# Optimization experiments

Measured on AMD Instinct MI355X. Metric: run time of the kernel, lower is better.

## Reference

```python
import jax, jax.numpy as jnp
import numpy as np

EPS = 1e-5
K = 32          # nsample in PCT sample_and_group
S1, S2 = 512, 256


def _bn_relu(h, gamma, beta, axes):
    # BatchNorm1d in training mode: batch stats over (batch, length) per channel (last axis here)
    mu = jnp.mean(h, axes, keepdims=True)
    var = jnp.var(h, axes, keepdims=True)
    return jax.nn.relu((h - mu) * jax.lax.rsqrt(var + EPS) * gamma + beta)


def _index_points(points, idx):
    # points [B,N,C], idx [B,...] int -> [B,...,C]
    return jax.vmap(lambda p, i: p[i])(points, idx)


def _fps(xyz, npoint):
    # farthest point sampling; deterministic start at index 0. xyz [B,N,3] -> [B,npoint] int32
    B, N, _ = xyz.shape

    def body(carry, _):
        dmin, far = carry
        c = jnp.take_along_axis(xyz, far[:, None, None], axis=1)  # [B,1,3]
        dmin = jnp.minimum(dmin, jnp.sum((xyz - c) ** 2, -1))     # [B,N]
        return (dmin, jnp.argmax(dmin, -1).astype(jnp.int32)), far

    init = (jnp.full((B, N), 1e10, xyz.dtype), jnp.zeros((B,), jnp.int32))
    _, idxs = jax.lax.scan(body, init, None, length=npoint)
    return jnp.transpose(idxs)  # [B, npoint]


def _sg(features, xyz, s, w1, g1, b1, w2, g2, b2):
    # features [B,N,C], xyz [B,N,3] -> (new_xyz [B,s,3], out [B,s,out_ch])
    xyz_c = jax.lax.stop_gradient(xyz)
    fps_idx = _fps(xyz_c, s)                       # [B,s]
    new_xyz = _index_points(xyz, fps_idx)          # [B,s,3]
    new_pts = _index_points(features, fps_idx)     # [B,s,C]
    q = jax.lax.stop_gradient(new_xyz)
    # squared distances centers->all points, [B,s,N]
    d = (jnp.sum(q * q, -1)[:, :, None] + jnp.sum(xyz_c * xyz_c, -1)[:, None, :]
         - 2.0 * jnp.einsum('bsc,bnc->bsn', q, xyz_c))
    _, knn = jax.lax.top_k(-d, K)                  # [B,s,K] nearest neighbors
    grouped = _index_points(features, knn)         # [B,s,K,C]
    rel = grouped - new_pts[:, :, None, :]
    feat = jnp.concatenate([rel, jnp.broadcast_to(new_pts[:, :, None, :], rel.shape)], -1)  # [B,s,K,2C]
    h = _bn_relu(jnp.einsum('bskc,oc->bsko', feat, w1), g1, b1, (0, 1, 2))
    h = _bn_relu(jnp.einsum('bskc,oc->bsko', h, w2), g2, b2, (0, 1, 2))
    return new_xyz, jnp.max(h, axis=2)             # max over K neighbors -> [B,s,out]


def _forward(x, w1, g1, b1, w2, g2, b2,
             s1_w1, s1_g1, s1_b1, s1_w2, s1_g2, s1_b2,
             s2_w1, s2_g1, s2_b1, s2_w2, s2_g2, s2_b2):
    xyz = jnp.transpose(x, (0, 2, 1))                                # [B,N,3]
    f = _bn_relu(jnp.einsum('bcn,oc->bno', x, w1), g1, b1, (0, 1))   # [B,N,64]
    f = _bn_relu(jnp.einsum('bnc,oc->bno', f, w2), g2, b2, (0, 1))   # [B,N,64]
    xyz1, f1 = _sg(f, xyz, S1, s1_w1, s1_g1, s1_b1, s1_w2, s1_g2, s1_b2)   # [B,512,128]
    _, f2 = _sg(f1, xyz1, S2, s2_w1, s2_g1, s2_b1, s2_w2, s2_g2, s2_b2)    # [B,256,256]
    return jnp.transpose(f2, (0, 2, 1))                              # [B,256,256] channel-first


def setup_inputs() -> dict:
    key = jax.random.key(0)
    ks = jax.random.split(key, 8)
    B, N = 32, 4096
    inp = {"x": jax.random.normal(ks[0], (B, 3, N), jnp.float32)}

    def w(k, o, i):
        return jax.random.normal(k, (o, i), jnp.float32) * (1.0 / np.sqrt(i))

    inp["w1"] = w(ks[1], 64, 3);   inp["g1"] = jnp.ones((64,), jnp.float32);  inp["b1"] = jnp.zeros((64,), jnp.float32)
    inp["w2"] = w(ks[2], 64, 64);  inp["g2"] = jnp.ones((64,), jnp.float32);  inp["b2"] = jnp.zeros((64,), jnp.float32)
    inp["s1_w1"] = w(ks[3], 128, 128); inp["s1_g1"] = jnp.ones((128,), jnp.float32); inp["s1_b1"] = jnp.zeros((128,), jnp.float32)
    inp["s1_w2"] = w(ks[4], 128, 128); inp["s1_g2"] = jnp.ones((128,), jnp.float32); inp["s1_b2"] = jnp.zeros((128,), jnp.float32)
    inp["s2_w1"] = w(ks[5], 256, 256); inp["s2_g1"] = jnp.ones((256,), jnp.float32); inp["s2_b1"] = jnp.zeros((256,), jnp.float32)
    inp["s2_w2"] = w(ks[6], 256, 256); inp["s2_g2"] = jnp.ones((256,), jnp.float32); inp["s2_b2"] = jnp.zeros((256,), jnp.float32)
    return inp


def reference(x, w1, g1, b1, w2, g2, b2,
              s1_w1, s1_g1, s1_b1, s1_w2, s1_g2, s1_b2,
              s2_w1, s2_g1, s2_b1, s2_w2, s2_g2, s2_b2):
    return _forward(x, w1, g1, b1, w2, g2, b2,
                    s1_w1, s1_g1, s1_b1, s1_w2, s1_g2, s1_b2,
                    s2_w1, s2_g1, s2_b1, s2_w2, s2_g2, s2_b2)
```

## Files before the change

kernel.cpp:

```cpp
#include <hip/hip_runtime.h>

typedef short short8 __attribute__((ext_vector_type(8)));
typedef _Float16 h8 __attribute__((ext_vector_type(8)));
typedef float f32x4 __attribute__((ext_vector_type(4)));

#define DEVI __device__ __forceinline__

DEVI float h2f(short s) { return (float)__builtin_bit_cast(_Float16, s); }
DEVI short f2h(float f) { return __builtin_bit_cast(short, (_Float16)f); }
DEVI f32x4 mfma16(short8 a, short8 b, f32x4 c) {
  return __builtin_amdgcn_mfma_f32_16x16x32_f16(
      __builtin_bit_cast(h8, a), __builtin_bit_cast(h8, b), c, 0, 0, 0);
}

DEVI float wave_max_bcast(float v) {
  const int ID = 0xff800000;
  int x = __builtin_bit_cast(int, v);
#define STEPM(ctrl)                                                     \
  {                                                                     \
    int t = __builtin_amdgcn_update_dpp(ID, x, ctrl, 0xf, 0xf, false);  \
    x = __builtin_bit_cast(int, fmaxf(__builtin_bit_cast(float, x),     \
                                      __builtin_bit_cast(float, t)));   \
  }
  STEPM(0x111) STEPM(0x112) STEPM(0x114) STEPM(0x118) STEPM(0x142) STEPM(0x143)
#undef STEPM
  return __builtin_bit_cast(float, __builtin_amdgcn_readlane(x, 63));
}
DEVI float wave_min_bcast_f(float v) {
  const int ID = 0x7f800000;
  int x = __builtin_bit_cast(int, v);
#define STEPN(ctrl)                                                     \
  {                                                                     \
    int t = __builtin_amdgcn_update_dpp(ID, x, ctrl, 0xf, 0xf, false);  \
    x = __builtin_bit_cast(int, fminf(__builtin_bit_cast(float, x),     \
                                      __builtin_bit_cast(float, t)));   \
  }
  STEPN(0x111) STEPN(0x112) STEPN(0x114) STEPN(0x118) STEPN(0x142) STEPN(0x143)
#undef STEPN
  return __builtin_bit_cast(float, __builtin_amdgcn_readlane(x, 63));
}
DEVI unsigned wave_min_bcast_u(unsigned v) {
  const int ID = (int)0xffffffff;
  int x = (int)v;
#define STEPU(ctrl)                                                     \
  {                                                                     \
    int t = __builtin_amdgcn_update_dpp(ID, x, ctrl, 0xf, 0xf, false);  \
    x = (int)((unsigned)x < (unsigned)t ? (unsigned)x : (unsigned)t);   \
  }
  STEPU(0x111) STEPU(0x112) STEPU(0x114) STEPU(0x118) STEPU(0x142) STEPU(0x143)
#undef STEPU
  return (unsigned)__builtin_amdgcn_readlane(x, 63);
}
DEVI unsigned wave_iscan_add(unsigned v) {
  int x = (int)v, t;
  t = __builtin_amdgcn_update_dpp(0, x, 0x111, 0xf, 0xf, false); x += t;
  t = __builtin_amdgcn_update_dpp(0, x, 0x112, 0xf, 0xf, false); x += t;
  t = __builtin_amdgcn_update_dpp(0, x, 0x114, 0xf, 0xf, false); x += t;
  t = __builtin_amdgcn_update_dpp(0, x, 0x118, 0xf, 0xf, false); x += t;
  t = __builtin_amdgcn_update_dpp(0, x, 0x142, 0xa, 0xf, false); x += t;
  t = __builtin_amdgcn_update_dpp(0, x, 0x143, 0xc, 0xf, false); x += t;
  return (unsigned)x;
}

__global__ __launch_bounds__(256) void prep_kernel(
    const float* __restrict__ w2, const float* __restrict__ s1w2,
    const float* __restrict__ s2w2, const float* __restrict__ s1w1,
    const float* __restrict__ s2w1, short* __restrict__ w2b,
    short* __restrict__ s1w2b, short* __restrict__ s2w2b,
    short* __restrict__ W1pp, short* __restrict__ W2pp) {
  int i = blockIdx.x * 256 + threadIdx.x;
  if (i < 4096) {
    w2b[i] = f2h(w2[i]);
  } else if (i < 20480) {
    int j = i - 4096; s1w2b[j] = f2h(s1w2[j]);
  } else if (i < 86016) {
    int j = i - 20480; s2w2b[j] = f2h(s2w2[j]);
  } else if (i < 102400) {
    int j = i - 86016; int c = j & 127;
    float v = s1w1[j]; if (c >= 64) v -= s1w1[j - 64];
    W1pp[j] = f2h(v);
  } else if (i < 167936) {
    int j = i - 102400; int c = j & 255;
    float v = s2w1[j]; if (c >= 128) v -= s2w1[j - 128];
    W2pp[j] = f2h(v);
  }
}

__global__ __launch_bounds__(256) void stageA_kernel(
    const float* __restrict__ x, const float* __restrict__ w1,
    float* __restrict__ xyz, short* __restrict__ h0) {
  int i = blockIdx.x * 256 + threadIdx.x;
  int b = i >> 12, n = i & 4095;
  const float* xb = x + ((size_t)b * 3 << 12) + n;
  float x0 = xb[0], x1 = xb[4096], x2 = xb[8192];
  float* xp = xyz + (size_t)i * 3;
  xp[0] = x0; xp[1] = x1; xp[2] = x2;
  short* hp = h0 + ((size_t)i << 6);
#pragma unroll
  for (int o8 = 0; o8 < 8; ++o8) {
    short8 t;
#pragma unroll
    for (int j = 0; j < 8; ++j) {
      int o = o8 * 8 + j;
      float h = x0 * w1[o * 3] + x1 * w1[o * 3 + 1] + x2 * w1[o * 3 + 2];
      t[j] = f2h(h);
    }
    *reinterpret_cast<short8*>(hp + o8 * 8) = t;
  }
}


DEVI void stats64_body(int bid, int nb, int tid, const short* __restrict__ h,
                       float* __restrict__ partials, int M) {
  __shared__ float l0[256], l1[256];
  const int c = tid & 63, g = tid >> 6;
  float s0 = 0.f, s1 = 0.f;
  for (int m = bid * 4 + g; m < M; m += nb * 4) {
    float v = h2f(h[(size_t)m * 64 + c]);
    s0 += v; s1 += v * v;
  }
  l0[tid] = s0; l1[tid] = s1;
  __syncthreads();
  if (g == 0) {
    for (int w = 1; w < 4; ++w) { s0 += l0[c + w * 64]; s1 += l1[c + w * 64]; }
    partials[(size_t)c * nb + bid] = s0;
    partials[(size_t)(64 + c) * nb + bid] = s1;
  }
}

DEVI void reduce2_body(int c, int tid, const float* __restrict__ partials,
                       const float* __restrict__ gamma, const float* __restrict__ beta,
                       float* __restrict__ scale, float* __restrict__ shift,
                       int NB, int C, float invM) {
  __shared__ float l0[4], l1[4];
  const float* p0 = partials + (size_t)c * NB;
  const float* p1 = partials + (size_t)(C + c) * NB;
  float s0 = 0.f, s1 = 0.f;
  for (int i = tid; i < NB; i += 256) { s0 += p0[i]; s1 += p1[i]; }
#pragma unroll
  for (int off = 1; off < 64; off <<= 1) {
    s0 += __shfl_xor(s0, off);
    s1 += __shfl_xor(s1, off);
  }
  if ((tid & 63) == 0) { l0[tid >> 6] = s0; l1[tid >> 6] = s1; }
  __syncthreads();
  if (tid == 0) {
    s0 = l0[0] + l0[1] + l0[2] + l0[3];
    s1 = l1[0] + l1[1] + l1[2] + l1[3];
    float mean = s0 * invM;
    float var = fmaxf(s1 * invM - mean * mean, 0.f);
    float sc = gamma[c] / sqrtf(var + 1e-5f);
    scale[c] = sc;
    shift[c] = beta[c] - mean * sc;
  }
}

__global__ __launch_bounds__(256) void reduce2_kernel(
    const float* __restrict__ partials, const float* __restrict__ gamma,
    const float* __restrict__ beta, float* __restrict__ scale,
    float* __restrict__ shift, int NB, int C, float invM) {
  reduce2_body(blockIdx.x, threadIdx.x, partials, gamma, beta, scale, shift, NB, C, invM);
}

DEVI void apply_body(int bid, int tid, const short* __restrict__ h,
                     short* __restrict__ f, const float* __restrict__ scale,
                     const float* __restrict__ shift) {
  size_t i = ((size_t)bid * 256 + tid) * 8;
  int c0 = (int)(i & 63);
  short8 v = *reinterpret_cast<const short8*>(h + i);
  short8 o;
#pragma unroll
  for (int j = 0; j < 8; ++j) {
    float y = h2f(v[j]) * scale[c0 + j] + shift[c0 + j];
    o[j] = f2h(fmaxf(y, 0.f));
  }
  *reinterpret_cast<short8*>(f + i) = o;
}

template <int NPTS, int T>
DEVI void fps_seg_body(char* smemraw, int bid, int tid, const float* __restrict__ xyz,
                       int* __restrict__ out, float* __restrict__ xyzc, int nsel,
                       int it0, int it1, float* __restrict__ dming,
                       int* __restrict__ farg) {
  __builtin_amdgcn_s_setprio(1);
  constexpr int PT = NPTS / T;
  constexpr int NW = T / 64;
  float* sx = (float*)smemraw;
  float* sy = sx + NPTS;
  float* sz = sy + NPTS;
  float* wv = sz + NPTS;
  unsigned* wi = (unsigned*)(wv + 2 * NW);
  const int lane = tid & 63, wave = tid >> 6;
  const float* base = xyz + (size_t)bid * NPTS * 3;
  float px[PT], py[PT], pz[PT], dmin[PT];
#pragma unroll
  for (int j = 0; j < PT; ++j) {
    int n = j * T + tid;
    px[j] = base[n * 3]; py[j] = base[n * 3 + 1]; pz[j] = base[n * 3 + 2];
    sx[n] = px[j]; sy[n] = py[j]; sz[n] = pz[j];
  }
  int far;
  if (it0 == 0) {
#pragma unroll
    for (int j = 0; j < PT; ++j) dmin[j] = 1e10f;
    far = 0;
  } else {
#pragma unroll
    for (int j = 0; j < PT; ++j) dmin[j] = dming[(size_t)bid * NPTS + j * T + tid];
    far = farg[bid];
  }
  __syncthreads();
  float cx = sx[far], cy = sy[far], cz = sz[far];
  for (int it = it0; it < it1; ++it) {
    if (tid == 0) {
      out[bid * nsel + it] = far;
      if (xyzc) {
        float* xc = xyzc + ((size_t)bid * nsel + it) * 3;
        xc[0] = cx; xc[1] = cy; xc[2] = cz;
      }
    }
    float bv = -1.f;
#pragma unroll
    for (int j = 0; j < PT; ++j) {
      float dx = __fsub_rn(px[j], cx), dy = __fsub_rn(py[j], cy), dz = __fsub_rn(pz[j], cz);
      float d = __fadd_rn(__fadd_rn(__fmul_rn(dx, dx), __fmul_rn(dy, dy)), __fmul_rn(dz, dz));
      float dm = fminf(dmin[j], d);
      dmin[j] = dm;
      bv = fmaxf(bv, dm);
    }
    float wmv = wave_max_bcast(bv);
    unsigned ci = 0xffffffffu;
#pragma unroll
    for (int j = PT - 1; j >= 0; --j)
      if (dmin[j] == wmv) ci = (unsigned)(j * T + tid);
    unsigned wmi = wave_min_bcast_u(ci);
    const int bsel = it & 1;
    if (lane == 0) { wv[bsel * NW + wave] = wmv; wi[bsel * NW + wave] = wmi; }
    __syncthreads();
    const int e = lane & (NW - 1);
    float v = wv[bsel * NW + e];
    unsigned si = wi[bsel * NW + e];
#define CMB(ctrl)                                                                        \
  {                                                                                      \
    float v2 = __builtin_bit_cast(                                                       \
        float, __builtin_amdgcn_update_dpp(0, __builtin_bit_cast(int, v), ctrl, 0xf, 0xf, true)); \
    unsigned i2 = (unsigned)__builtin_amdgcn_update_dpp(0, (int)si, ctrl, 0xf, 0xf, true);\
    bool bt = (v2 > v) || (v2 == v && i2 < si);                                          \
    v = bt ? v2 : v; si = bt ? i2 : si;                                                  \
  }
    if constexpr (NW >= 2) CMB(0x121)
    if constexpr (NW >= 4) CMB(0x122)
    if constexpr (NW >= 8) CMB(0x124)
#undef CMB
    far = (int)si;
    cx = sx[far]; cy = sy[far]; cz = sz[far];
  }
  if (it1 < nsel) {
#pragma unroll
    for (int j = 0; j < PT; ++j) dming[(size_t)bid * NPTS + j * T + tid] = dmin[j];
    if (tid == 0) farg[bid] = far;
  }
}

#define KNN_SMEM_BYTES ((4096 + 256 + 4 + 256 + 256) * 4)
template <int NPTS, int S>
DEVI void knn_body(char* smemraw, int bs, int tid, const float* __restrict__ pts,
                   const int* __restrict__ fpsidx, int* __restrict__ knn) {
  constexpr int PT = NPTS / 256;
  unsigned* hist = (unsigned*)smemraw;
  unsigned* csums = hist + 4096;
  unsigned* meta = csums + 256;
  float* bval = (float*)(meta + 4);
  unsigned* bidx = (unsigned*)(bval + 256);
  const int lane = tid & 63, wave = tid >> 6;
  const int b = bs / S;
  const int cidx = fpsidx[bs];
  const float* cp = pts + ((size_t)b * NPTS + cidx) * 3;
  const float qx = cp[0], qy = cp[1], qz = cp[2];
  const float qq = __fadd_rn(__fadd_rn(__fmul_rn(qx, qx), __fmul_rn(qy, qy)), __fmul_rn(qz, qz));
  const float* base = pts + (size_t)b * NPTS * 3;
  float d[PT]; unsigned u[PT];
#pragma unroll
  for (int j = 0; j < PT; ++j) {
    int n = j * 256 + tid;
    float x = base[n * 3], y = base[n * 3 + 1], z = base[n * 3 + 2];
    float pp = __fadd_rn(__fadd_rn(__fmul_rn(x, x), __fmul_rn(y, y)), __fmul_rn(z, z));
    float dot = __fadd_rn(__fadd_rn(__fmul_rn(qx, x), __fmul_rn(qy, y)), __fmul_rn(qz, z));
    d[j] = __fsub_rn(__fadd_rn(qq, pp), __fmul_rn(2.f, dot));
    unsigned bits = __builtin_bit_cast(unsigned, d[j]);
    unsigned m = (unsigned)((int)bits >> 31);
    u[j] = bits ^ (m | 0x80000000u);
  }
  {
    uint4 z4 = {0u, 0u, 0u, 0u};
    uint4* hq = (uint4*)hist;
    for (int i = tid; i < 1024; i += 256) hq[i] = z4;
    if (tid == 0) { meta[0] = 0; meta[3] = 0; }
  }
  __syncthreads();
#pragma unroll
  for (int j = 0; j < PT; ++j) atomicAdd(&hist[u[j] >> 20], 1u);
  __syncthreads();
  {
    const uint4* hq = (const uint4*)(hist + tid * 16);
    unsigned cs = 0;
#pragma unroll
    for (int q = 0; q < 4; ++q) {
      uint4 v = hq[q];
      cs += v.x + v.y + v.z + v.w;
    }
    csums[tid] = cs;
  }
  __syncthreads();
  if (wave == 0) {
    const int t4 = lane * 4;
    unsigned c0 = csums[t4], c1 = csums[t4 + 1], c2 = csums[t4 + 2], c3 = csums[t4 + 3];
    unsigned lt = c0 + c1 + c2 + c3;
    unsigned incl = wave_iscan_add(lt);
    unsigned excl = incl - lt;
    unsigned long long blt = __ballot(incl >= 32u);
    int L = __ffsll((long long)blt) - 1;
    if (lane == L) {
      unsigned cum = excl;
      int bucket = -1;
      unsigned cc[4] = {c0, c1, c2, c3};
#pragma unroll
      for (int q = 0; q < 4; ++q) {
        if (bucket < 0 && cum + cc[q] >= 32u) {
          int bbase = (t4 + q) * 16;
          for (int h = 0; h < 16; ++h) {
            unsigned hv = hist[bbase + h];
            if (cum + hv >= 32u) { bucket = bbase + h; break; }
            cum += hv;
          }
        } else if (bucket < 0) {
          cum += cc[q];
        }
      }
      meta[1] = (unsigned)bucket;
      meta[2] = cum;
    }
  }
  __syncthreads();
  const unsigned B = meta[1];
  const unsigned cb = meta[2];
  int* kout = knn + (size_t)bs * 32;
#pragma unroll
  for (int j = 0; j < PT; ++j) {
    unsigned bk = u[j] >> 20;
    if (bk < B) {
      unsigned p = atomicAdd(&meta[0], 1u);
      kout[p] = j * 256 + tid;
    } else if (bk == B) {
      unsigned p = atomicAdd(&meta[3], 1u);
      if (p < 256u) { bval[p] = d[j]; bidx[p] = (unsigned)(j * 256 + tid); }
    }
  }
  __syncthreads();
  const int m = 32 - (int)cb;
  if (wave == 0 && m > 0) {
    unsigned nb = meta[3]; if (nb > 256u) nb = 256u;
    float v0 = (lane < (int)nb) ? bval[lane] : 3.4e38f;
    unsigned i0 = (lane < (int)nb) ? bidx[lane] : 0xffffffffu;
    float v1 = (lane + 64 < (int)nb) ? bval[lane + 64] : 3.4e38f;
    unsigned i1 = (lane + 64 < (int)nb) ? bidx[lane + 64] : 0xffffffffu;
    float v2 = (lane + 128 < (int)nb) ? bval[lane + 128] : 3.4e38f;
    unsigned i2 = (lane + 128 < (int)nb) ? bidx[lane + 128] : 0xffffffffu;
    float v3 = (lane + 192 < (int)nb) ? bval[lane + 192] : 3.4e38f;
    unsigned i3 = (lane + 192 < (int)nb) ? bidx[lane + 192] : 0xffffffffu;
    for (int k = 0; k < m; ++k) {
      float lv = v0; unsigned li = i0;
      if (v1 < lv || (v1 == lv && i1 < li)) { lv = v1; li = i1; }
      if (v2 < lv || (v2 == lv && i2 < li)) { lv = v2; li = i2; }
      if (v3 < lv || (v3 == lv && i3 < li)) { lv = v3; li = i3; }
      float wmv = wave_min_bcast_f(lv);
      unsigned ci = (lv == wmv) ? li : 0xffffffffu;
      unsigned wmi = wave_min_bcast_u(ci);
      if (lane == 0) kout[cb + k] = (int)wmi;
      if (i0 == wmi) { v0 = 3.4e38f; i0 = 0xffffffffu; }
      if (i1 == wmi) { v1 = 3.4e38f; i1 = 0xffffffffu; }
      if (i2 == wmi) { v2 = 3.4e38f; i2 = 0xffffffffu; }
      if (i3 == wmi) { v3 = 3.4e38f; i3 = 0xffffffffu; }
    }
  }
}

template <int KD, int ND, bool GATHER, bool BNA, int NPTS, int S>
DEVI void gemm_body(char* smemraw, int bid, int tid, int gemmBlocks,
                    const short* A, const int* KNNp, const int* FPSp,
                    const short* __restrict__ W, const float* __restrict__ bnscale,
                    const float* __restrict__ bnshift, short* Hout,
                    float* __restrict__ partials) {
  constexpr int C = KD / 2;
  constexpr int NT = (ND > 128) ? 8 : ND / 16;
  constexpr int BR = (ND > 128) ? 64 : 128;
  constexpr int KC = (ND >= 256) ? 64 : KD;
  constexpr int LOG2KC = (KC == 64) ? 6 : 7;
  constexpr int NCH = KD / KC;
  constexpr int KTC = KC / 32;
  constexpr int LROW = KC + 8;
  short* lb = (short*)smemraw;
  float* lstats = (float*)(smemraw + ND * LROW * 2);
  const int wave = tid >> 6, lane = tid & 63;
  const int rowOff = (ND > 128) ? (wave >> 1) * 32 : wave * 32;
  const int colOff = (ND > 128) ? (wave & 1) * 128 : 0;
  const int mBase = bid * BR + rowOff;
  for (int i = tid; i < 2 * ND; i += 256) lstats[i] = 0.f;

  const short* aptr[2][2];
#pragma unroll
  for (int rg = 0; rg < 2; ++rg) {
    int m = mBase + rg * 16 + (lane & 15);
    if constexpr (GATHER) {
      int idx = KNNp[m];
      int bb = m / (S * 32);
      int s = (m - bb * (S * 32)) >> 5;
      int fidx = FPSp[bb * S + s];
      aptr[rg][0] = A + ((size_t)bb * NPTS + idx) * C;
      aptr[rg][1] = A + ((size_t)bb * NPTS + fidx) * C;
    } else {
      aptr[rg][0] = A + (size_t)m * KD;
      aptr[rg][1] = A + (size_t)m * KD + C;
    }
  }
  const int koLane = (lane >> 4) * 8;
  f32x4 acc[2][NT];
#pragma unroll
  for (int rg = 0; rg < 2; ++rg)
#pragma unroll
    for (int nt = 0; nt < NT; ++nt) acc[rg][nt] = (f32x4){0.f, 0.f, 0.f, 0.f};

#pragma unroll
  for (int ch = 0; ch < NCH; ++ch) {
    __syncthreads();
    constexpr int SIT = (ND * KC) / 2048;
#pragma unroll
    for (int i = 0; i < SIT; ++i) {
      int e = i * 2048 + tid * 8;
      int n = e >> LOG2KC, kk = e & (KC - 1);
      short8 v = *reinterpret_cast<const short8*>(W + (size_t)n * KD + ch * KC + kk);
      *reinterpret_cast<short8*>(&lb[n * LROW + kk]) = v;
    }
    __syncthreads();
#pragma unroll
    for (int ktc = 0; ktc < KTC; ++ktc) {
      const int kt = ch * KTC + ktc;
      const int half = (kt * 32 >= C) ? 1 : 0;
      const int ko = kt * 32 + koLane;
      const int koh = ko - half * C;
      short8 afrag[2];
#pragma unroll
      for (int rg = 0; rg < 2; ++rg) {
        short8 a = *reinterpret_cast<const short8*>(aptr[rg][half] + koh);
        if constexpr (BNA) {
          const float* scp = bnscale + ko;
          const float* shp = bnshift + ko;
#pragma unroll
          for (int j = 0; j < 8; ++j) {
            float v = h2f(a[j]);
            v = fmaxf(v * scp[j] + shp[j], 0.f);
            a[j] = f2h(v);
          }
        }
        afrag[rg] = a;
      }
#pragma unroll
      for (int nt = 0; nt < NT; ++nt) {
        short8 bfr = *reinterpret_cast<const short8*>(
            &lb[(colOff + nt * 16 + (lane & 15)) * LROW + ktc * 32 + koLane]);
        acc[0][nt] = mfma16(afrag[0], bfr, acc[0][nt]);
        acc[1][nt] = mfma16(afrag[1], bfr, acc[1][nt]);
      }
    }
  }
  __syncthreads();

#pragma unroll
  for (int nt = 0; nt < NT; ++nt) {
    float s0 = 0.f, s1 = 0.f;
#pragma unroll
    for (int rg = 0; rg < 2; ++rg)
#pragma unroll
      for (int i = 0; i < 4; ++i) {
        float v = acc[rg][nt][i];
        s0 += v; s1 += v * v;
      }
    s0 += __shfl_xor(s0, 16); s0 += __shfl_xor(s0, 32);
    s1 += __shfl_xor(s1, 16); s1 += __shfl_xor(s1, 32);
    if (lane < 16) {
      atomicAdd(&lstats[colOff + nt * 16 + lane], s0);
      atomicAdd(&lstats[ND + colOff + nt * 16 + lane], s1);
    }
  }
#pragma unroll
  for (int rg = 0; rg < 2; ++rg)
#pragma unroll
    for (int nt = 0; nt < NT; ++nt)
#pragma unroll
      for (int i = 0; i < 4; ++i) {
        int m2 = mBase + rg * 16 + (lane >> 4) * 4 + i;
        int n = colOff + nt * 16 + (lane & 15);
        Hout[(size_t)m2 * ND + n] = f2h(acc[rg][nt][i]);
      }
  __syncthreads();
  for (int i = tid; i < 2 * ND; i += 256)
    partials[(size_t)i * gemmBlocks + bid] = lstats[i];
}


template <int FN, int FT>
__global__ __launch_bounds__(256, 1) void fps_stats_seg(
    int fpsBlocks, const float* fxyz, int* fout, float* fxyzc, int fnsel,
    int it0, int it1, float* dming, int* farg,
    const short* sh, float* sp, int sM, int snb) {
  extern __shared__ char smem[];
  if ((int)blockIdx.x < fpsBlocks)
    fps_seg_body<FN, FT>(smem, blockIdx.x, threadIdx.x, fxyz, fout, fxyzc, fnsel,
                         it0, it1, dming, farg);
  else
    stats64_body(blockIdx.x - fpsBlocks, snb, threadIdx.x, sh, sp, sM);
}

template <int FN, int FT>
__global__ __launch_bounds__(256, 1) void fps_r2_seg(
    int fpsBlocks, const float* fxyz, int* fout, float* fxyzc, int fnsel,
    int it0, int it1, float* dming, int* farg,
    const float* partials, const float* gamma, const float* beta,
    float* scale, float* shift, int NB, int C, float invM) {
  extern __shared__ char smem[];
  if ((int)blockIdx.x < fpsBlocks)
    fps_seg_body<FN, FT>(smem, blockIdx.x, threadIdx.x, fxyz, fout, fxyzc, fnsel,
                         it0, it1, dming, farg);
  else
    reduce2_body(blockIdx.x - fpsBlocks, threadIdx.x, partials, gamma, beta, scale,
                 shift, NB, C, invM);
}

template <int FN, int FT, int KD, int ND, bool BNA>
__global__ __launch_bounds__(256, 1) void fps_gemm_seg(
    int fpsBlocks, const float* fxyz, int* fout, float* fxyzc, int fnsel,
    int it0, int it1, float* dming, int* farg,
    const short* A, const short* W, const float* bnscale, const float* bnshift,
    short* Hout, float* partials) {
  extern __shared__ char smem[];
  if ((int)blockIdx.x < fpsBlocks)
    fps_seg_body<FN, FT>(smem, blockIdx.x, threadIdx.x, fxyz, fout, fxyzc, fnsel,
                         it0, it1, dming, farg);
  else
    gemm_body<KD, ND, false, BNA, 1, 1>(smem, blockIdx.x - fpsBlocks, threadIdx.x,
                                        gridDim.x - fpsBlocks, A, nullptr, nullptr,
                                        W, bnscale, bnshift, Hout, partials);
}

template <int FN, int FT>
__global__ __launch_bounds__(256, 1) void fps_apply_seg(
    int fpsBlocks, const float* fxyz, int* fout, float* fxyzc, int fnsel,
    int it0, int it1, float* dming, int* farg,
    const short* ah, short* af, const float* ascale, const float* ashift) {
  extern __shared__ char smem[];
  if ((int)blockIdx.x < fpsBlocks)
    fps_seg_body<FN, FT>(smem, blockIdx.x, threadIdx.x, fxyz, fout, fxyzc, fnsel,
                         it0, it1, dming, farg);
  else
    apply_body(blockIdx.x - fpsBlocks, threadIdx.x, ah, af, ascale, ashift);
}

template <int KD, int ND, bool BNA, int FN, int FT>
__global__ __launch_bounds__(256, 1) void gemm_fps_kernel(
    int fpsBlocks, const short* A, const short* W, const float* bnscale,
    const float* bnshift, short* Hout, float* partials,
    const float* fxyz, int* fout, float* fxyzc, int fnsel) {
  extern __shared__ char smem[];
  if ((int)blockIdx.x < fpsBlocks)
    fps_seg_body<FN, FT>(smem, blockIdx.x, threadIdx.x, fxyz, fout, fxyzc, fnsel,
                         0, fnsel, nullptr, nullptr);
  else
    gemm_body<KD, ND, false, BNA, 1, 1>(smem, blockIdx.x - fpsBlocks, threadIdx.x,
                                        gridDim.x - fpsBlocks, A, nullptr, nullptr,
                                        W, bnscale, bnshift, Hout, partials);
}

template <int KD, int ND, bool GATHER, bool BNA, int NPTS, int S>
__global__ __launch_bounds__(256, 2) void gemm_kernel(
    const short* A, const int* KNNp, const int* FPSp, const short* W,
    const float* bnscale, const float* bnshift, short* Hout, float* partials) {
  extern __shared__ char smem[];
  gemm_body<KD, ND, GATHER, BNA, NPTS, S>(smem, blockIdx.x, threadIdx.x, gridDim.x,
                                          A, KNNp, FPSp, W, bnscale, bnshift, Hout,
                                          partials);
}

template <int NPTS, int S>
__global__ __launch_bounds__(256, 4) void knn_kernel2(
    const float* pts, const int* fpsidx, int* knn) {
  __shared__ __align__(16) char smem[KNN_SMEM_BYTES];
  knn_body<NPTS, S>(smem, blockIdx.x, threadIdx.x, pts, fpsidx, knn);
}

template <int NPTS, int S>
__global__ __launch_bounds__(256, 4) void maxpool_knn_kernel(
    int knnBlocks, const float* pts, const int* fpsidx, int* knn,
    const short* h, const float* scale, const float* shift, short* f1) {
  __shared__ __align__(16) char smem[KNN_SMEM_BYTES];
  if ((int)blockIdx.x < knnBlocks) {
    knn_body<NPTS, S>(smem, blockIdx.x, threadIdx.x, pts, fpsidx, knn);
  } else {
    const int bs = (blockIdx.x - knnBlocks) * 2 + (threadIdx.x >> 7);
    const int c = threadIdx.x & 127;
    const float sc = scale[c], sh = shift[c];
    float m = 0.f;
    for (int k = 0; k < 32; ++k) {
      float v = h2f(h[((size_t)bs * 32 + k) * 128 + c]);
      m = fmaxf(m, fmaxf(v * sc + sh, 0.f));
    }
    f1[(size_t)bs * 128 + c] = f2h(m);
  }
}

__global__ __launch_bounds__(256) void maxpool_out_kernel(
    const short* __restrict__ h, const float* __restrict__ scale,
    const float* __restrict__ shift, float* __restrict__ out) {
  const int bs = blockIdx.x, c = threadIdx.x;
  const int b = bs >> 8, s = bs & 255;
  const float sc = scale[c], sh = shift[c];
  float m = 0.f;
  for (int k = 0; k < 32; ++k) {
    float v = h2f(h[((size_t)bs * 32 + k) * 256 + c]);
    m = fmaxf(m, fmaxf(v * sc + sh, 0.f));
  }
  out[((size_t)b << 16) + ((size_t)c << 8) + s] = m;
}

extern "C" void kernel_launch(void* const* d_in, const int* in_sizes, int n_in,
                              void* d_out, int out_size, void* d_ws, size_t ws_size,
                              hipStream_t stream) {
  (void)in_sizes; (void)n_in; (void)out_size; (void)ws_size;
  const float* x    = (const float*)d_in[0];
  const float* w1   = (const float*)d_in[1];
  const float* g1   = (const float*)d_in[2];
  const float* b1   = (const float*)d_in[3];
  const float* w2   = (const float*)d_in[4];
  const float* g2   = (const float*)d_in[5];
  const float* b2   = (const float*)d_in[6];
  const float* s1w1 = (const float*)d_in[7];
  const float* s1g1 = (const float*)d_in[8];
  const float* s1b1 = (const float*)d_in[9];
  const float* s1w2 = (const float*)d_in[10];
  const float* s1g2 = (const float*)d_in[11];
  const float* s1b2 = (const float*)d_in[12];
  const float* s2w1 = (const float*)d_in[13];
  const float* s2g1 = (const float*)d_in[14];
  const float* s2b1 = (const float*)d_in[15];
  const float* s2w2 = (const float*)d_in[16];
  const float* s2g2 = (const float*)d_in[17];
  const float* s2b2 = (const float*)d_in[18];
  float* out = (float*)d_out;

  char* ws = (char*)d_ws;
  size_t off = 0;
  auto alloc = [&](size_t bytes) -> char* {
    size_t p = (off + 255) & ~(size_t)255;
    off = p + bytes;
    return ws + p;
  };

  float* xyz      = (float*)alloc(32ull * 4096 * 3 * 4);
  short* h0       = (short*)alloc(32ull * 4096 * 64 * 2);
  short* hb       = (short*)alloc(32ull * 4096 * 64 * 2);
  short* fb       = (short*)alloc(32ull * 4096 * 64 * 2);
  int*   fps1     = (int*)alloc(32ull * 512 * 4);
  float* xyzc1    = (float*)alloc(32ull * 512 * 3 * 4);
  int*   knn1     = (int*)alloc(32ull * 512 * 32 * 4);
  short* f1       = (short*)alloc(32ull * 512 * 128 * 2);
  int*   fps2     = (int*)alloc(32ull * 256 * 4);
  int*   knn2     = (int*)alloc(32ull * 256 * 32 * 4);
  float* dming    = (float*)alloc(32ull * 4096 * 4);
  int*   farg     = (int*)alloc(32 * 4);
  short* hbuf     = (short*)alloc(134217728ull);
  float* partials = (float*)alloc(2ull * 256 * 4096 * 4);
  float* scA  = (float*)alloc(64 * 4);  float* shA  = (float*)alloc(64 * 4);
  float* scBc = (float*)alloc(64 * 4);  float* shBc = (float*)alloc(64 * 4);
  float* sc1a = (float*)alloc(128 * 4); float* sh1a = (float*)alloc(128 * 4);
  float* sc1b = (float*)alloc(128 * 4); float* sh1b = (float*)alloc(128 * 4);
  float* sc2a = (float*)alloc(256 * 4); float* sh2a = (float*)alloc(256 * 4);
  float* sc2b = (float*)alloc(256 * 4); float* sh2b = (float*)alloc(256 * 4);
  short* w2b   = (short*)alloc(4096 * 2);
  short* s1w2b = (short*)alloc(16384 * 2);
  short* s2w2b = (short*)alloc(65536 * 2);
  short* W1pp  = (short*)alloc(16384 * 2);
  short* W2pp  = (short*)alloc(65536 * 2);

  prep_kernel<<<656, 256, 0, stream>>>(w2, s1w2, s2w2, s1w1, s2w1, w2b, s1w2b, s2w2b, W1pp, W2pp);
  stageA_kernel<<<512, 256, 0, stream>>>(x, w1, xyz, h0);

  fps_stats_seg<4096, 256><<<288, 256, 49216, stream>>>(
      32, xyz, fps1, xyzc1, 512, 0, 103, dming, farg, h0, partials, 131072, 256);
  fps_r2_seg<4096, 256><<<96, 256, 49216, stream>>>(
      32, xyz, fps1, xyzc1, 512, 103, 205, dming, farg,
      partials, g1, b1, scA, shA, 256, 64, 1.f / 131072.f);
  fps_gemm_seg<4096, 256, 64, 64, true><<<1056, 256, 49216, stream>>>(
      32, xyz, fps1, xyzc1, 512, 205, 308, dming, farg,
      h0, w2b, scA, shA, hb, partials);
  fps_r2_seg<4096, 256><<<96, 256, 49216, stream>>>(
      32, xyz, fps1, xyzc1, 512, 308, 410, dming, farg,
      partials, g2, b2, scBc, shBc, 1024, 64, 1.f / 131072.f);
  fps_apply_seg<4096, 256><<<4128, 256, 49216, stream>>>(
      32, xyz, fps1, xyzc1, 512, 410, 512, dming, farg, hb, fb, scBc, shBc);

  knn_kernel2<4096, 512><<<16384, 256, 0, stream>>>(xyz, fps1, knn1);

  gemm_kernel<128, 128, true, false, 4096, 512><<<4096, 256, 35840, stream>>>(
      fb, knn1, fps1, W1pp, nullptr, nullptr, hbuf, partials);
  reduce2_kernel<<<128, 256, 0, stream>>>(partials, s1g1, s1b1, sc1a, sh1a, 4096, 128, 1.f / 524288.f);

  gemm_fps_kernel<128, 128, true, 512, 256><<<4128, 256, 35840, stream>>>(
      32, hbuf, s1w2b, sc1a, sh1a, hbuf, partials, xyzc1, fps2, nullptr, 256);
  reduce2_kernel<<<128, 256, 0, stream>>>(partials, s1g2, s1b2, sc1b, sh1b, 4096, 128, 1.f / 524288.f);

  maxpool_knn_kernel<512, 256><<<16384, 256, 0, stream>>>(
      8192, xyzc1, fps2, knn2, hbuf, sc1b, sh1b, f1);

  gemm_kernel<256, 256, true, false, 512, 256><<<4096, 256, 38912, stream>>>(
      f1, knn2, fps2, W2pp, nullptr, nullptr, hbuf, partials);
  reduce2_kernel<<<256, 256, 0, stream>>>(partials, s2g1, s2b1, sc2a, sh2a, 4096, 256, 1.f / 262144.f);
  gemm_kernel<256, 256, false, true, 1, 1><<<4096, 256, 38912, stream>>>(
      hbuf, nullptr, nullptr, s2w2b, sc2a, sh2a, hbuf, partials);
  reduce2_kernel<<<256, 256, 0, stream>>>(partials, s2g2, s2b2, sc2b, sh2b, 4096, 256, 1.f / 262144.f);
  maxpool_out_kernel<<<8192, 256, 0, stream>>>(hbuf, sc2b, sh2b, out);
}
```

Measured before the change: 942.1 us.

## Fuse neighbor max/min pooling into second GEMM epilogue; stage stores via LDS

The second GEMM of each set-abstraction stage no longer writes the full [B,s,K,C] pre-BN activation. It reduces max and min over the 32 neighbours in registers and writes only per-center max/min in fp32. Because BN is affine per channel, the pooling kernels pick max or min by the sign of the scale and then apply BN+ReLU, which removes a large write and re-read of hbuf. The other GEMMs now stage output through LDS so global stores are coalesced 16-byte vectors, at the cost of an extra shared-memory pass and a barrier.

```diff
diff --git a/kernel.cpp b/kernel.cpp
--- a/kernel.cpp
+++ b/kernel.cpp
@@ -385,11 +385,12 @@
   }
 }
 
-template <int KD, int ND, bool GATHER, bool BNA, int NPTS, int S>
+template <int KD, int ND, bool GATHER, bool BNA, int NPTS, int S, int EPI>
 DEVI void gemm_body(char* smemraw, int bid, int tid, int gemmBlocks,
                     const short* A, const int* KNNp, const int* FPSp,
                     const short* __restrict__ W, const float* __restrict__ bnscale,
                     const float* __restrict__ bnshift, short* Hout,
+                    float* __restrict__ mmax, float* __restrict__ mmin,
                     float* __restrict__ partials) {
   constexpr int C = KD / 2;
   constexpr int NT = (ND > 128) ? 8 : ND / 16;
@@ -399,8 +400,12 @@
   constexpr int NCH = KD / KC;
   constexpr int KTC = KC / 32;
   constexpr int LROW = KC + 8;
+  constexpr int TROW = ND + 8;
+  constexpr int LBB = ND * LROW * 2;
+  constexpr int TBB = BR * TROW * 2;
+  constexpr int LSOFF = (LBB > TBB) ? LBB : TBB;
   short* lb = (short*)smemraw;
-  float* lstats = (float*)(smemraw + ND * LROW * 2);
+  float* lstats = (float*)(smemraw + LSOFF);
   const int wave = tid >> 6, lane = tid & 63;
   const int rowOff = (ND > 128) ? (wave >> 1) * 32 : wave * 32;
   const int colOff = (ND > 128) ? (wave & 1) * 128 : 0;
@@ -492,17 +497,49 @@
       atomicAdd(&lstats[ND + colOff + nt * 16 + lane], s1);
     }
   }
-#pragma unroll
-  for (int rg = 0; rg < 2; ++rg)
-#pragma unroll
-    for (int nt = 0; nt < NT; ++nt)
-#pragma unroll
-      for (int i = 0; i < 4; ++i) {
-        int m2 = mBase + rg * 16 + (lane >> 4) * 4 + i;
-        int n = colOff + nt * 16 + (lane & 15);
-        Hout[(size_t)m2 * ND + n] = f2h(acc[rg][nt][i]);
+
+  if constexpr (EPI == 0) {
+#pragma unroll
+    for (int rg = 0; rg < 2; ++rg)
+#pragma unroll
+      for (int nt = 0; nt < NT; ++nt)
+#pragma unroll
+        for (int i = 0; i < 4; ++i) {
+          int r = rowOff + rg * 16 + (lane >> 4) * 4 + i;
+          int n = colOff + nt * 16 + (lane & 15);
+          lb[r * TROW + n] = f2h(acc[rg][nt][i]);
+        }
+    __syncthreads();
+    constexpr int TPR = ND / 8;
+    constexpr int RPI = 256 / TPR;
+    const int r0 = tid / TPR, c0 = (tid % TPR) * 8;
+#pragma unroll
+    for (int it = 0; it < BR / RPI; ++it) {
+      int r = it * RPI + r0;
+      short8 v = *reinterpret_cast<const short8*>(&lb[r * TROW + c0]);
+      *reinterpret_cast<short8*>(&Hout[(size_t)(bid * BR + r) * ND + c0]) = v;
+    }
+  } else {
+    const int center = (bid * BR + rowOff) >> 5;
+#pragma unroll
+    for (int nt = 0; nt < NT; ++nt) {
+      float mx = -3.4e38f, mn = 3.4e38f;
+#pragma unroll
+      for (int rg = 0; rg < 2; ++rg)
+#pragma unroll
+        for (int i = 0; i < 4; ++i) {
+          float v = acc[rg][nt][i];
+          mx = fmaxf(mx, v); mn = fminf(mn, v);
+        }
+      mx = fmaxf(mx, __shfl_xor(mx, 16)); mx = fmaxf(mx, __shfl_xor(mx, 32));
+      mn = fminf(mn, __shfl_xor(mn, 16)); mn = fminf(mn, __shfl_xor(mn, 32));
+      if (lane < 16) {
+        mmax[(size_t)center * ND + colOff + nt * 16 + lane] = mx;
+        mmin[(size_t)center * ND + colOff + nt * 16 + lane] = mn;
       }
-  __syncthreads();
+    }
+    __syncthreads();
+  }
   for (int i = tid; i < 2 * ND; i += 256)
     partials[(size_t)i * gemmBlocks + bid] = lstats[i];
 }
@@ -536,20 +573,21 @@
                  shift, NB, C, invM);
 }
 
-template <int FN, int FT, int KD, int ND, bool BNA>
+template <int FN, int FT, int KD, int ND, bool BNA, int EPI>
 __global__ __launch_bounds__(256, 1) void fps_gemm_seg(
     int fpsBlocks, const float* fxyz, int* fout, float* fxyzc, int fnsel,
     int it0, int it1, float* dming, int* farg,
     const short* A, const short* W, const float* bnscale, const float* bnshift,
-    short* Hout, float* partials) {
+    short* Hout, float* mmax, float* mmin, float* partials) {
   extern __shared__ char smem[];
   if ((int)blockIdx.x < fpsBlocks)
     fps_seg_body<FN, FT>(smem, blockIdx.x, threadIdx.x, fxyz, fout, fxyzc, fnsel,
                          it0, it1, dming, farg);
   else
-    gemm_body<KD, ND, false, BNA, 1, 1>(smem, blockIdx.x - fpsBlocks, threadIdx.x,
-                                        gridDim.x - fpsBlocks, A, nullptr, nullptr,
-                                        W, bnscale, bnshift, Hout, partials);
+    gemm_body<KD, ND, false, BNA, 1, 1, EPI>(smem, blockIdx.x - fpsBlocks, threadIdx.x,
+                                             gridDim.x - fpsBlocks, A, nullptr, nullptr,
+                                             W, bnscale, bnshift, Hout, mmax, mmin,
+                                             partials);
 }
 
 template <int FN, int FT>
@@ -565,29 +603,31 @@
     apply_body(blockIdx.x - fpsBlocks, threadIdx.x, ah, af, ascale, ashift);
 }
 
-template <int KD, int ND, bool BNA, int FN, int FT>
+template <int KD, int ND, bool BNA, int EPI, int FN, int FT>
 __global__ __launch_bounds__(256, 1) void gemm_fps_kernel(
     int fpsBlocks, const short* A, const short* W, const float* bnscale,
-    const float* bnshift, short* Hout, float* partials,
+    const float* bnshift, short* Hout, float* mmax, float* mmin, float* partials,
     const float* fxyz, int* fout, float* fxyzc, int fnsel) {
   extern __shared__ char smem[];
   if ((int)blockIdx.x < fpsBlocks)
     fps_seg_body<FN, FT>(smem, blockIdx.x, threadIdx.x, fxyz, fout, fxyzc, fnsel,
                          0, fnsel, nullptr, nullptr);
   else
-    gemm_body<KD, ND, false, BNA, 1, 1>(smem, blockIdx.x - fpsBlocks, threadIdx.x,
-                                        gridDim.x - fpsBlocks, A, nullptr, nullptr,
-                                        W, bnscale, bnshift, Hout, partials);
-}
-
-template <int KD, int ND, bool GATHER, bool BNA, int NPTS, int S>
+    gemm_body<KD, ND, false, BNA, 1, 1, EPI>(smem, blockIdx.x - fpsBlocks, threadIdx.x,
+                                             gridDim.x - fpsBlocks, A, nullptr, nullptr,
+                                             W, bnscale, bnshift, Hout, mmax, mmin,
+                                             partials);
+}
+
+template <int KD, int ND, bool GATHER, bool BNA, int NPTS, int S, int EPI>
 __global__ __launch_bounds__(256, 2) void gemm_kernel(
     const short* A, const int* KNNp, const int* FPSp, const short* W,
-    const float* bnscale, const float* bnshift, short* Hout, float* partials) {
+    const float* bnscale, const float* bnshift, short* Hout,
+    float* mmax, float* mmin, float* partials) {
   extern __shared__ char smem[];
-  gemm_body<KD, ND, GATHER, BNA, NPTS, S>(smem, blockIdx.x, threadIdx.x, gridDim.x,
-                                          A, KNNp, FPSp, W, bnscale, bnshift, Hout,
-                                          partials);
+  gemm_body<KD, ND, GATHER, BNA, NPTS, S, EPI>(smem, blockIdx.x, threadIdx.x,
+                                               gridDim.x, A, KNNp, FPSp, W, bnscale,
+                                               bnshift, Hout, mmax, mmin, partials);
 }
 
 template <int NPTS, int S>
@@ -600,35 +640,29 @@
 template <int NPTS, int S>
 __global__ __launch_bounds__(256, 4) void maxpool_knn_kernel(
     int knnBlocks, const float* pts, const int* fpsidx, int* knn,
-    const short* h, const float* scale, const float* shift, short* f1) {
+    const float* mmax, const float* mmin, const float* scale, const float* shift,
+    short* f1) {
   __shared__ __align__(16) char smem[KNN_SMEM_BYTES];
   if ((int)blockIdx.x < knnBlocks) {
     knn_body<NPTS, S>(smem, blockIdx.x, threadIdx.x, pts, fpsidx, knn);
   } else {
-    const int bs = (blockIdx.x - knnBlocks) * 2 + (threadIdx.x >> 7);
+    const int ctr = (blockIdx.x - knnBlocks) * 2 + (threadIdx.x >> 7);
     const int c = threadIdx.x & 127;
     const float sc = scale[c], sh = shift[c];
-    float m = 0.f;
-    for (int k = 0; k < 32; ++k) {
-      float v = h2f(h[((size_t)bs * 32 + k) * 128 + c]);
-      m = fmaxf(m, fmaxf(v * sc + sh, 0.f));
-    }
-    f1[(size_t)bs * 128 + c] = f2h(m);
+    float y = (sc >= 0.f) ? mmax[(size_t)ctr * 128 + c] : mmin[(size_t)ctr * 128 + c];
+    f1[(size_t)ctr * 128 + c] = f2h(fmaxf(sc * y + sh, 0.f));
   }
 }
 
 __global__ __launch_bounds__(256) void maxpool_out_kernel(
-    const short* __restrict__ h, const float* __restrict__ scale,
-    const float* __restrict__ shift, float* __restrict__ out) {
+    const float* __restrict__ mmax, const float* __restrict__ mmin,
+    const float* __restrict__ scale, const float* __restrict__ shift,
+    float* __restrict__ out) {
   const int bs = blockIdx.x, c = threadIdx.x;
   const int b = bs >> 8, s = bs & 255;
   const float sc = scale[c], sh = shift[c];
-  float m = 0.f;
-  for (int k = 0; k < 32; ++k) {
-    float v = h2f(h[((size_t)bs * 32 + k) * 256 + c]);
-    m = fmaxf(m, fmaxf(v * sc + sh, 0.f));
-  }
-  out[((size_t)b << 16) + ((size_t)c << 8) + s] = m;
+  float y = (sc >= 0.f) ? mmax[(size_t)bs * 256 + c] : mmin[(size_t)bs * 256 + c];
+  out[((size_t)b << 16) + ((size_t)c << 8) + s] = fmaxf(sc * y + sh, 0.f);
 }
 
 extern "C" void kernel_launch(void* const* d_in, const int* in_sizes, int n_in,
@@ -677,6 +711,10 @@
   float* dming    = (float*)alloc(32ull * 4096 * 4);
   int*   farg     = (int*)alloc(32 * 4);
   short* hbuf     = (short*)alloc(134217728ull);
+  float* mm1max   = (float*)alloc(16384ull * 128 * 4);
+  float* mm1min   = (float*)alloc(16384ull * 128 * 4);
+  float* mm2max   = (float*)alloc(8192ull * 256 * 4);
+  float* mm2min   = (float*)alloc(8192ull * 256 * 4);
   float* partials = (float*)alloc(2ull * 256 * 4096 * 4);
   float* scA  = (float*)alloc(64 * 4);  float* shA  = (float*)alloc(64 * 4);
   float* scBc = (float*)alloc(64 * 4);  float* shBc = (float*)alloc(64 * 4);
@@ -698,9 +736,9 @@
   fps_r2_seg<4096, 256><<<96, 256, 49216, stream>>>(
       32, xyz, fps1, xyzc1, 512, 103, 205, dming, farg,
       partials, g1, b1, scA, shA, 256, 64, 1.f / 131072.f);
-  fps_gemm_seg<4096, 256, 64, 64, true><<<1056, 256, 49216, stream>>>(
+  fps_gemm_seg<4096, 256, 64, 64, true, 0><<<1056, 256, 49216, stream>>>(
       32, xyz, fps1, xyzc1, 512, 205, 308, dming, farg,
-      h0, w2b, scA, shA, hb, partials);
+      h0, w2b, scA, shA, hb, nullptr, nullptr, partials);
   fps_r2_seg<4096, 256><<<96, 256, 49216, stream>>>(
       32, xyz, fps1, xyzc1, 512, 308, 410, dming, farg,
       partials, g2, b2, scBc, shBc, 1024, 64, 1.f / 131072.f);
@@ -709,22 +747,23 @@
 
   knn_kernel2<4096, 512><<<16384, 256, 0, stream>>>(xyz, fps1, knn1);
 
-  gemm_kernel<128, 128, true, false, 4096, 512><<<4096, 256, 35840, stream>>>(
-      fb, knn1, fps1, W1pp, nullptr, nullptr, hbuf, partials);
+  gemm_kernel<128, 128, true, false, 4096, 512, 0><<<4096, 256, 35840, stream>>>(
+      fb, knn1, fps1, W1pp, nullptr, nullptr, hbuf, nullptr, nullptr, partials);
   reduce2_kernel<<<128, 256, 0, stream>>>(partials, s1g1, s1b1, sc1a, sh1a, 4096, 128, 1.f / 524288.f);
 
-  gemm_fps_kernel<128, 128, true, 512, 256><<<4128, 256, 35840, stream>>>(
-      32, hbuf, s1w2b, sc1a, sh1a, hbuf, partials, xyzc1, fps2, nullptr, 256);
+  gemm_fps_kernel<128, 128, true, 1, 512, 256><<<4128, 256, 35840, stream>>>(
+      32, hbuf, s1w2b, sc1a, sh1a, nullptr, mm1max, mm1min, partials,
+      xyzc1, fps2, nullptr, 256);
   reduce2_kernel<<<128, 256, 0, stream>>>(partials, s1g2, s1b2, sc1b, sh1b, 4096, 128, 1.f / 524288.f);
 
   maxpool_knn_kernel<512, 256><<<16384, 256, 0, stream>>>(
-      8192, xyzc1, fps2, knn2, hbuf, sc1b, sh1b, f1);
-
-  gemm_kernel<256, 256, true, false, 512, 256><<<4096, 256, 38912, stream>>>(
-      f1, knn2, fps2, W2pp, nullptr, nullptr, hbuf, partials);
+      8192, xyzc1, fps2, knn2, mm1max, mm1min, sc1b, sh1b, f1);
+
+  gemm_kernel<256, 256, true, false, 512, 256, 0><<<4096, 256, 38912, stream>>>(
+      f1, knn2, fps2, W2pp, nullptr, nullptr, hbuf, nullptr, nullptr, partials);
   reduce2_kernel<<<256, 256, 0, stream>>>(partials, s2g1, s2b1, sc2a, sh2a, 4096, 256, 1.f / 262144.f);
-  gemm_kernel<256, 256, false, true, 1, 1><<<4096, 256, 38912, stream>>>(
-      hbuf, nullptr, nullptr, s2w2b, sc2a, sh2a, hbuf, partials);
+  gemm_kernel<256, 256, false, true, 1, 1, 1><<<4096, 256, 38912, stream>>>(
+      hbuf, nullptr, nullptr, s2w2b, sc2a, sh2a, nullptr, mm2max, mm2min, partials);
   reduce2_kernel<<<256, 256, 0, stream>>>(partials, s2g2, s2b2, sc2b, sh2b, 4096, 256, 1.f / 262144.f);
-  maxpool_out_kernel<<<8192, 256, 0, stream>>>(hbuf, sc2b, sh2b, out);
-}
+  maxpool_out_kernel<<<8192, 256, 0, stream>>>(mm2max, mm2min, sc2b, sh2b, out);
+}
```

New measurement: 932.4 us. Within noise of the previous version (-1.0%).
